# Kernel tuning notes

Hardware: AMD Instinct MI355X
Metric: run time of the kernel (lower is better)

## Reference

```python
import jax, jax.numpy as jnp
import numpy as np

D_MODEL = 768
D_STATE = 128
D_CONV = 4
EXPAND = 4
D_INNER = EXPAND * D_MODEL  # 3072
DT_RANK = 48  # ceil(768/16), mamba default dt_rank='auto'
H_MLP = 768
EPS = 1e-6


def setup_inputs() -> dict:
    key = jax.random.key(0)
    ks = jax.random.split(key, 12)
    B, T = 1, 384

    def rn(k, shape, s=0.02):
        return jax.random.normal(k, shape, jnp.float32) * s

    inp = {}
    inp["x"] = jax.random.normal(ks[0], (B, 3 * T, D_MODEL), jnp.float32)
    inp["ln_w"] = jnp.ones((6, D_MODEL), jnp.float32)  # ln1..ln6 RMSNorm weights
    # 3 independent Mamba blocks, params stacked on leading dim
    inp["in_proj_w"] = rn(ks[1], (3, 2 * D_INNER, D_MODEL))
    inp["conv_w"] = rn(ks[2], (3, D_INNER, 1, D_CONV), 0.1)  # depthwise causal conv1d
    inp["conv_b"] = rn(ks[3], (3, D_INNER), 0.1)
    inp["x_proj_w"] = rn(ks[4], (3, DT_RANK + 2 * D_STATE, D_INNER))
    inp["dt_proj_w"] = rn(ks[5], (3, D_INNER, DT_RANK), 0.1)
    inp["dt_proj_b"] = rn(ks[6], (3, D_INNER), 0.1) - 4.0  # small dt after softplus
    A = jnp.tile(jnp.arange(1, D_STATE + 1, dtype=jnp.float32)[None, None, :], (3, D_INNER, 1))
    inp["A_log"] = jnp.log(A)  # mamba S4D-real init
    inp["D_skip"] = jnp.ones((3, D_INNER), jnp.float32)
    inp["out_proj_w"] = rn(ks[7], (3, D_MODEL, D_INNER))
    # 3 GatedMLPs: fc1 -> 2*hidden (value, gate), silu gate, fc2 -> out
    inp["fc1_w"] = rn(ks[8], (3, 2 * H_MLP, D_MODEL))
    inp["fc1_b"] = jnp.zeros((3, 2 * H_MLP), jnp.float32)
    inp["fc2_w"] = rn(ks[9], (3, D_MODEL, H_MLP))
    inp["fc2_b"] = jnp.zeros((3, D_MODEL), jnp.float32)
    return inp


def _rmsnorm(x, w):
    v = jnp.mean(jnp.square(x), axis=-1, keepdims=True)
    return x * jax.lax.rsqrt(v + EPS) * w


def _mamba(u, in_w, cw, cb, xp_w, dt_w, dt_b, A_log, D_skip, out_w):
    # u: (B, T, D_MODEL)
    Bsz = u.shape[0]
    xz = u @ in_w.T  # (B,T,2*Di)
    x, z = jnp.split(xz, 2, axis=-1)
    # causal depthwise conv1d over time
    xc = jax.lax.conv_general_dilated(
        jnp.swapaxes(x, 1, 2), cw, (1,), [(D_CONV - 1, 0)],
        feature_group_count=D_INNER)  # (B,Di,T)
    x = jax.nn.silu(jnp.swapaxes(xc, 1, 2) + cb)  # (B,T,Di)
    x_dbl = x @ xp_w.T  # (B,T,dt_rank+2N)
    dt = x_dbl[..., :DT_RANK]
    Bm = x_dbl[..., DT_RANK:DT_RANK + D_STATE]
    Cm = x_dbl[..., DT_RANK + D_STATE:]
    delta = jax.nn.softplus(dt @ dt_w.T + dt_b)  # (B,T,Di)
    A = -jnp.exp(A_log)  # (Di,N)

    def step(h, inp):
        d_t, B_t, C_t, u_t = inp  # (B,Di),(B,N),(B,N),(B,Di)
        h = jnp.exp(d_t[:, :, None] * A) * h + (d_t * u_t)[:, :, None] * B_t[:, None, :]
        y = jnp.einsum('bdn,bn->bd', h, C_t)
        return h, y

    h0 = jnp.zeros((Bsz, D_INNER, D_STATE), u.dtype)
    xs = tuple(jnp.swapaxes(a, 0, 1) for a in (delta, Bm, Cm, x))  # time-major
    _, ys = jax.lax.scan(jax.checkpoint(step), h0, xs)
    y = jnp.swapaxes(ys, 0, 1) + x * D_skip  # (B,T,Di)
    return (y * jax.nn.silu(z)) @ out_w.T  # (B,T,D_MODEL)


def _gmlp(x, w1, b1, w2, b2):
    h = x @ w1.T + b1
    a, g = jnp.split(h, 2, axis=-1)
    return (jax.nn.silu(g) * a) @ w2.T + b2


def reference(x, ln_w, in_proj_w, conv_w, conv_b, x_proj_w, dt_proj_w, dt_proj_b,
              A_log, D_skip, out_proj_w, fc1_w, fc1_b, fc2_w, fc2_b):
    t = x.shape[1] // 3
    outs = []
    for i in range(3):  # music / up / down branches
        b = x[:, i * t:(i + 1) * t]
        b = b + _mamba(_rmsnorm(b, ln_w[2 * i]), in_proj_w[i], conv_w[i], conv_b[i],
                       x_proj_w[i], dt_proj_w[i], dt_proj_b[i], A_log[i], D_skip[i],
                       out_proj_w[i])
        b = b + _gmlp(_rmsnorm(b, ln_w[2 * i + 1]), fc1_w[i], fc1_b[i], fc2_w[i], fc2_b[i])
        outs.append(b)
    return jnp.concatenate(outs, axis=1)
```

## Files before the change

### kernel.cpp

```cpp
#include <hip/hip_runtime.h>
#include <hip/hip_bf16.h>

#define TSEQ 384
#define DMODEL 768
#define DINNER 3072
#define DSTATE 128
#define DTRANK 48
#define XPROJ_N (DTRANK + 2*DSTATE)
#define NSEG 3
#define LOG2E 1.44269504088896340736f
#define LN2F  0.69314718055994530942f

typedef __attribute__((ext_vector_type(8))) short short8;
typedef __attribute__((ext_vector_type(4))) float floatx4;
typedef unsigned short u16;
typedef unsigned int u32;

__device__ __forceinline__ float bf2f(u16 u) {
    return __uint_as_float(((unsigned)u) << 16);
}
__device__ __forceinline__ float ldf(const void* p, size_t i, int bf) {
    return bf ? bf2f(((const u16*)p)[i]) : ((const float*)p)[i];
}
__device__ __forceinline__ void stf(void* p, size_t i, float v, int bf) {
    if (bf) ((__hip_bfloat16*)p)[i] = __float2bfloat16(v);
    else    ((float*)p)[i] = v;
}
__device__ __forceinline__ float silu_f(float v) { return v / (1.f + __expf(-v)); }
__device__ __forceinline__ u16 f2bf(float f) {
    unsigned u = __float_as_uint(f);
    return (u16)((u + 0x7FFFu + ((u >> 16) & 1u)) >> 16);
}

__device__ __forceinline__ float exp2_fast(float x) {
#if __has_builtin(__builtin_amdgcn_exp2f)
    return __builtin_amdgcn_exp2f(x);
#else
    return exp2f(x);
#endif
}

template<int CTRL>
__device__ __forceinline__ float ror_add(float x) {
    int r = __builtin_amdgcn_update_dpp(0, __float_as_int(x), CTRL, 0xF, 0xF, true);
    return x + __int_as_float(r);
}

__device__ __forceinline__ void gl16(const void* g, void* l) {
    __builtin_amdgcn_global_load_lds(
        (const __attribute__((address_space(1))) u32*)g,
        (__attribute__((address_space(3))) u32*)l, 16, 0, 0);
}

__global__ void k_detect(const unsigned* lnw_bits, int* flag) {
    if (threadIdx.x == 0) {
        flag[0] = (lnw_bits[0] == 0x3F803F80u) ? 1 : 0;
    }
}

__global__ __launch_bounds__(256) void k_rmsnorm(
    const void* src, int src_is_f32, const void* lnw, int wbase,
    u16* out, const int* flagp)
{
    int bf  = *flagp;
    int sbf = src_is_f32 ? 0 : bf;
    int r   = blockIdx.x;
    int seg = r / TSEQ;
    int wrow = 2*seg + wbase;
    int tid = threadIdx.x;
    float v[3]; float s = 0.f;
    #pragma unroll
    for (int j = 0; j < 3; ++j) {
        int e = j*256 + tid;
        v[j] = ldf(src, (size_t)r*DMODEL + e, sbf);
        s += v[j]*v[j];
    }
    __shared__ float red[256];
    red[tid] = s; __syncthreads();
    for (int st = 128; st > 0; st >>= 1) {
        if (tid < st) red[tid] += red[tid+st];
        __syncthreads();
    }
    float rs = rsqrtf(red[0]/(float)DMODEL + 1e-6f);
    #pragma unroll
    for (int j = 0; j < 3; ++j) {
        int e = j*256 + tid;
        out[(size_t)r*DMODEL + e] = f2bf(v[j]*rs*ldf(lnw, (size_t)wrow*DMODEL + e, bf));
    }
}

__global__ __launch_bounds__(256) void k_gemm(
    const float* A, const void* W, const void* bias,
    float* C, const int* flagp, int M, int N, int K, int lda)
{
    int bf  = *flagp;
    int seg = blockIdx.z;
    int mbase = blockIdx.y * 64, nbase = blockIdx.x * 64;
    int tid = threadIdx.x;
    int tx = tid & 15, ty = tid >> 4;

    __shared__ float As[16][68];
    __shared__ float Ws[16][68];

    const float* Ag = A + (size_t)seg*M*lda;
    size_t segW = (size_t)seg*N*K;

    int lrow = tid >> 2;
    int lk   = (tid & 3) * 4;
    int wn   = nbase + lrow;

    float acc[4][4];
    #pragma unroll
    for (int i = 0; i < 4; ++i)
        #pragma unroll
        for (int j = 0; j < 4; ++j) acc[i][j] = 0.f;

    for (int kt = 0; kt < K; kt += 16) {
        float4 av = *reinterpret_cast<const float4*>(Ag + (size_t)(mbase+lrow)*lda + kt + lk);
        As[lk+0][lrow] = av.x; As[lk+1][lrow] = av.y;
        As[lk+2][lrow] = av.z; As[lk+3][lrow] = av.w;
        float w0=0.f, w1=0.f, w2=0.f, w3=0.f;
        if (wn < N) {
            size_t off = segW + (size_t)wn*K + kt + lk;
            if (bf) {
                ushort4 q = *reinterpret_cast<const ushort4*>((const u16*)W + off);
                w0 = bf2f(q.x); w1 = bf2f(q.y); w2 = bf2f(q.z); w3 = bf2f(q.w);
            } else {
                float4 f = *reinterpret_cast<const float4*>((const float*)W + off);
                w0 = f.x; w1 = f.y; w2 = f.z; w3 = f.w;
            }
        }
        Ws[lk+0][lrow] = w0; Ws[lk+1][lrow] = w1;
        Ws[lk+2][lrow] = w2; Ws[lk+3][lrow] = w3;
        __syncthreads();
        #pragma unroll
        for (int kk = 0; kk < 16; ++kk) {
            float4 a4 = *reinterpret_cast<const float4*>(&As[kk][ty*4]);
            float4 b4 = *reinterpret_cast<const float4*>(&Ws[kk][tx*4]);
            float ar[4] = {a4.x, a4.y, a4.z, a4.w};
            float br[4] = {b4.x, b4.y, b4.z, b4.w};
            #pragma unroll
            for (int i = 0; i < 4; ++i)
                #pragma unroll
                for (int j = 0; j < 4; ++j)
                    acc[i][j] = fmaf(ar[i], br[j], acc[i][j]);
        }
        __syncthreads();
    }

    #pragma unroll
    for (int i = 0; i < 4; ++i) {
        int m = mbase + ty*4 + i;
        #pragma unroll
        for (int j = 0; j < 4; ++j) {
            int n = nbase + tx*4 + j;
            if (n < N) {
                float v = acc[i][j] + ldf(bias, (size_t)seg*N + n, bf);
                v = (v > 20.f) ? v : log1pf(__expf(v));
                C[((size_t)(seg*M + m))*N + n] = v;
            }
        }
    }
}

#define LPITCH 40
__global__ __launch_bounds__(256) void k_gemm_mfma128(
    const u16* A, const void* W, u16* C, const int* flagp,
    int M, int N, int K)
{
    int bf  = *flagp;
    int seg = blockIdx.z;
    int mbase = blockIdx.y * 128, nbase = blockIdx.x * 128;
    int tid = threadIdx.x;
    int w = tid >> 6, lane = tid & 63;
    int wm = w >> 1, wn = w & 1;
    int quad = lane >> 4, l16 = lane & 15;

    __shared__ short As[128 * LPITCH];
    __shared__ short Ws[128 * LPITCH];

    const u16* Ag = A + (size_t)seg*M*K + (size_t)mbase*K;
    size_t segW = (size_t)seg*N*K;

    int sr  = tid >> 1;
    int skc = (tid & 1) * 16;

    floatx4 acc[4][4];
    #pragma unroll
    for (int i = 0; i < 4; ++i)
        #pragma unroll
        for (int j = 0; j < 4; ++j)
            acc[i][j] = (floatx4){0.f, 0.f, 0.f, 0.f};

    int wrow = nbase + sr;
    for (int kt = 0; kt < K; kt += 32) {
        const u16* ap = Ag + (size_t)sr*K + kt + skc;
        *reinterpret_cast<short8*>(&As[sr*LPITCH + skc])     = *reinterpret_cast<const short8*>(ap);
        *reinterpret_cast<short8*>(&As[sr*LPITCH + skc + 8]) = *reinterpret_cast<const short8*>(ap + 8);
        {
            short8 s0 = (short8){0,0,0,0,0,0,0,0}, s1 = s0;
            if (wrow < N) {
                size_t off = segW + (size_t)wrow*K + kt + skc;
                if (bf) {
                    s0 = *reinterpret_cast<const short8*>((const u16*)W + off);
                    s1 = *reinterpret_cast<const short8*>((const u16*)W + off + 8);
                } else {
                    const float* wp = (const float*)W + off;
                    float f[16];
                    #pragma unroll
                    for (int q = 0; q < 4; ++q) {
                        float4 v = *reinterpret_cast<const float4*>(wp + q*4);
                        f[q*4+0] = v.x; f[q*4+1] = v.y; f[q*4+2] = v.z; f[q*4+3] = v.w;
                    }
                    #pragma unroll
                    for (int q = 0; q < 8; ++q) { s0[q] = (short)f2bf(f[q]); s1[q] = (short)f2bf(f[q+8]); }
                }
            }
            *reinterpret_cast<short8*>(&Ws[sr*LPITCH + skc])     = s0;
            *reinterpret_cast<short8*>(&Ws[sr*LPITCH + skc + 8]) = s1;
        }
        __syncthreads();
        short8 af[4], bfr[4];
        #pragma unroll
        for (int i = 0; i < 4; ++i)
            af[i] = *reinterpret_cast<const short8*>(&As[(wm*64 + i*16 + l16)*LPITCH + quad*8]);
        #pragma unroll
        for (int j = 0; j < 4; ++j)
            bfr[j] = *reinterpret_cast<const short8*>(&Ws[(wn*64 + j*16 + l16)*LPITCH + quad*8]);
        #pragma unroll
        for (int i = 0; i < 4; ++i)
            #pragma unroll
            for (int j = 0; j < 4; ++j)
                acc[i][j] = __builtin_amdgcn_mfma_f32_16x16x32_bf16(af[i], bfr[j], acc[i][j], 0, 0, 0);
        __syncthreads();
    }

    #pragma unroll
    for (int i = 0; i < 4; ++i) {
        #pragma unroll
        for (int reg = 0; reg < 4; ++reg) {
            int grow = mbase + wm*64 + i*16 + quad*4 + reg;
            #pragma unroll
            for (int j = 0; j < 4; ++j) {
                int gcol = nbase + wn*64 + j*16 + l16;
                if (gcol < N)
                    C[((size_t)(seg*M + grow))*N + gcol] = f2bf(acc[i][j][reg]);
            }
        }
    }
}

#define LP2 72
__global__ __launch_bounds__(256) void k_gemm_mfma64(
    const u16* A, const void* W, const void* bias, const void* resid,
    int resid_flagged, void* C, int c_mode, const int* flagp,
    int M, int N, int K)
{
    int bf  = *flagp;
    int seg = blockIdx.z;
    int mbase = blockIdx.y * 64, nbase = blockIdx.x * 64;
    int tid = threadIdx.x;
    int w = tid >> 6, lane = tid & 63;
    int wm = w >> 1, wn = w & 1;
    int quad = lane >> 4, l16 = lane & 15;

    __shared__ short As[64 * LP2];
    __shared__ short Ws[64 * LP2];

    const u16* Ag = A + (size_t)seg*M*K + (size_t)mbase*K;
    size_t segW = (size_t)seg*N*K;

    int sr  = tid >> 2;
    int skc = (tid & 3) * 16;

    floatx4 acc[2][2];
    #pragma unroll
    for (int i = 0; i < 2; ++i)
        #pragma unroll
        for (int j = 0; j < 2; ++j)
            acc[i][j] = (floatx4){0.f, 0.f, 0.f, 0.f};

    int wrow = nbase + sr;
    for (int kt = 0; kt < K; kt += 64) {
        const u16* ap = Ag + (size_t)sr*K + kt + skc;
        *reinterpret_cast<short8*>(&As[sr*LP2 + skc])     = *reinterpret_cast<const short8*>(ap);
        *reinterpret_cast<short8*>(&As[sr*LP2 + skc + 8]) = *reinterpret_cast<const short8*>(ap + 8);
        {
            short8 s0 = (short8){0,0,0,0,0,0,0,0}, s1 = s0;
            if (wrow < N) {
                size_t off = segW + (size_t)wrow*K + kt + skc;
                if (bf) {
                    s0 = *reinterpret_cast<const short8*>((const u16*)W + off);
                    s1 = *reinterpret_cast<const short8*>((const u16*)W + off + 8);
                } else {
                    const float* wp = (const float*)W + off;
                    float f[16];
                    #pragma unroll
                    for (int q = 0; q < 4; ++q) {
                        float4 v = *reinterpret_cast<const float4*>(wp + q*4);
                        f[q*4+0] = v.x; f[q*4+1] = v.y; f[q*4+2] = v.z; f[q*4+3] = v.w;
                    }
                    #pragma unroll
                    for (int q = 0; q < 8; ++q) { s0[q] = (short)f2bf(f[q]); s1[q] = (short)f2bf(f[q+8]); }
                }
            }
            *reinterpret_cast<short8*>(&Ws[sr*LP2 + skc])     = s0;
            *reinterpret_cast<short8*>(&Ws[sr*LP2 + skc + 8]) = s1;
        }
        __syncthreads();
        #pragma unroll
        for (int kk = 0; kk < 2; ++kk) {
            short8 af[2], bfr[2];
            #pragma unroll
            for (int i = 0; i < 2; ++i)
                af[i] = *reinterpret_cast<const short8*>(&As[(wm*32 + i*16 + l16)*LP2 + kk*32 + quad*8]);
            #pragma unroll
            for (int j = 0; j < 2; ++j)
                bfr[j] = *reinterpret_cast<const short8*>(&Ws[(wn*32 + j*16 + l16)*LP2 + kk*32 + quad*8]);
            #pragma unroll
            for (int i = 0; i < 2; ++i)
                #pragma unroll
                for (int j = 0; j < 2; ++j)
                    acc[i][j] = __builtin_amdgcn_mfma_f32_16x16x32_bf16(af[i], bfr[j], acc[i][j], 0, 0, 0);
        }
        __syncthreads();
    }

    #pragma unroll
    for (int i = 0; i < 2; ++i) {
        #pragma unroll
        for (int reg = 0; reg < 4; ++reg) {
            int grow = mbase + wm*32 + i*16 + quad*4 + reg;
            #pragma unroll
            for (int j = 0; j < 2; ++j) {
                int gcol = nbase + wn*32 + j*16 + l16;
                if (gcol < N) {
                    float v = acc[i][j][reg];
                    if (bias) v += ldf(bias, (size_t)seg*N + gcol, bf);
                    size_t idx = ((size_t)(seg*M + grow))*N + gcol;
                    if (resid) v += resid_flagged ? ldf(resid, idx, bf)
                                                  : ((const float*)resid)[idx];
                    if      (c_mode == 0) ((float*)C)[idx] = v;
                    else if (c_mode == 1) ((u16*)C)[idx] = f2bf(v);
                    else                  stf(C, idx, v, bf);
                }
            }
        }
    }
}

__global__ __launch_bounds__(256) void k_fc1_gate(
    const u16* A, const void* W, const void* bias, u16* act, const int* flagp)
{
    const int M = TSEQ, K = DMODEL, NF = 2*DMODEL;
    int bf  = *flagp;
    int seg = blockIdx.z;
    int mbase = blockIdx.y * 64, nbase = blockIdx.x * 64;
    int tid = threadIdx.x;
    int w = tid >> 6, lane = tid & 63;
    int wm = w >> 1, wn = w & 1;
    int quad = lane >> 4, l16 = lane & 15;

    __shared__ short As[64 * LPITCH];
    __shared__ short Wa[64 * LPITCH];
    __shared__ short Wg[64 * LPITCH];

    const u16* Ag = A + (size_t)seg*M*K + (size_t)mbase*K;
    size_t segW = (size_t)seg*NF*K;

    int sr  = tid >> 2;
    int skc = (tid & 3) * 8;

    floatx4 acca[2][2], accg[2][2];
    #pragma unroll
    for (int i = 0; i < 2; ++i)
        #pragma unroll
        for (int j = 0; j < 2; ++j) {
            acca[i][j] = (floatx4){0.f, 0.f, 0.f, 0.f};
            accg[i][j] = (floatx4){0.f, 0.f, 0.f, 0.f};
        }

    int wra = nbase + sr;
    int wrg = nbase + DMODEL + sr;
    for (int kt = 0; kt < K; kt += 32) {
        *reinterpret_cast<short8*>(&As[sr*LPITCH + skc]) =
            *reinterpret_cast<const short8*>(Ag + (size_t)sr*K + kt + skc);
        #pragma unroll
        for (int half = 0; half < 2; ++half) {
            int wrow = half ? wrg : wra;
            short* dst = half ? Wg : Wa;
            short8 s;
            size_t off = segW + (size_t)wrow*K + kt + skc;
            if (bf) {
                s = *reinterpret_cast<const short8*>((const u16*)W + off);
            } else {
                const float* wp = (const float*)W + off;
                float4 v0 = *reinterpret_cast<const float4*>(wp);
                float4 v1 = *reinterpret_cast<const float4*>(wp + 4);
                s[0]=(short)f2bf(v0.x); s[1]=(short)f2bf(v0.y); s[2]=(short)f2bf(v0.z); s[3]=(short)f2bf(v0.w);
                s[4]=(short)f2bf(v1.x); s[5]=(short)f2bf(v1.y); s[6]=(short)f2bf(v1.z); s[7]=(short)f2bf(v1.w);
            }
            *reinterpret_cast<short8*>(&dst[sr*LPITCH + skc]) = s;
        }
        __syncthreads();
        short8 af[2], ba[2], bg[2];
        #pragma unroll
        for (int i = 0; i < 2; ++i)
            af[i] = *reinterpret_cast<const short8*>(&As[(wm*32 + i*16 + l16)*LPITCH + quad*8]);
        #pragma unroll
        for (int j = 0; j < 2; ++j) {
            ba[j] = *reinterpret_cast<const short8*>(&Wa[(wn*32 + j*16 + l16)*LPITCH + quad*8]);
            bg[j] = *reinterpret_cast<const short8*>(&Wg[(wn*32 + j*16 + l16)*LPITCH + quad*8]);
        }
        #pragma unroll
        for (int i = 0; i < 2; ++i)
            #pragma unroll
            for (int j = 0; j < 2; ++j) {
                acca[i][j] = __builtin_amdgcn_mfma_f32_16x16x32_bf16(af[i], ba[j], acca[i][j], 0, 0, 0);
                accg[i][j] = __builtin_amdgcn_mfma_f32_16x16x32_bf16(af[i], bg[j], accg[i][j], 0, 0, 0);
            }
        __syncthreads();
    }

    #pragma unroll
    for (int i = 0; i < 2; ++i) {
        #pragma unroll
        for (int reg = 0; reg < 4; ++reg) {
            int grow = mbase + wm*32 + i*16 + quad*4 + reg;
            #pragma unroll
            for (int j = 0; j < 2; ++j) {
                int gcol = nbase + wn*32 + j*16 + l16;
                float va = acca[i][j][reg] + ldf(bias, (size_t)seg*NF + gcol, bf);
                float vg = accg[i][j][reg] + ldf(bias, (size_t)seg*NF + DMODEL + gcol, bf);
                act[((size_t)(seg*M + grow))*DMODEL + gcol] = f2bf(va * silu_f(vg));
            }
        }
    }
}

__global__ __launch_bounds__(256) void k_conv(
    const u16* xz, const void* cw, const void* cb, u16* xconv, const int* flagp)
{
    int bf = *flagp;
    size_t gid = (size_t)blockIdx.x*256 + threadIdx.x;
    int d = (int)(gid % DINNER);
    size_t rt = gid / DINNER;
    int t = (int)(rt % TSEQ);
    int seg = (int)(rt / TSEQ);
    float acc = ldf(cb, (size_t)seg*DINNER + d, bf);
    const u16* xs = xz + (size_t)seg*TSEQ*(2*DINNER);
    #pragma unroll
    for (int j = 0; j < 4; ++j) {
        int ts = t - 3 + j;
        if (ts >= 0)
            acc = fmaf(ldf(cw, ((size_t)seg*DINNER + d)*4 + j, bf),
                       bf2f(xs[(size_t)ts*(2*DINNER) + d]), acc);
    }
    xconv[gid] = f2bf(silu_f(acc));
}

#define WSCH 4
#define WSCT 8
#define NPAIR (TSEQ/(2*WSCT))
#define NBX   (DINNER/WSCH)
#define GUARD_TH 0.04f

__global__ __launch_bounds__(64) void k_scan_wave(
    const float* delta, const u16* xconv, const float* xdbl, const u16* xz,
    const void* A_log, const void* D_skip, u16* yout, const int* flagp)
{
    int bf   = flagp[0];
    int seg  = blockIdx.y;
    int bx = (int)blockIdx.x;
    bx = (bx & 7) * (NBX/8) + (bx >> 3);
    int dbase = bx * WSCH;
    int lane = threadIdx.x;
    int ch = lane >> 4, sl = lane & 15;
    int d = dbase + ch;

    __shared__ float4 BUF[2][WSCT][64];
    __shared__ float  DLB2[WSCT][8];

    float a[8];
    size_t abase = ((size_t)seg*DINNER + d)*DSTATE + (size_t)sl*8;
    #pragma unroll
    for (int j = 0; j < 8; ++j)
        a[j] = -__expf(ldf(A_log, abase + j, bf)) * LOG2E;
    float gl[8]; float gmax = 0.f;
    gl[0] = 0.f;
    #pragma unroll
    for (int j = 1; j < 8; ++j) {
        gl[j] = (a[j] - a[j-1]) * LN2F;
        gmax = fmaxf(gmax, fabsf(gl[j]));
    }
    float wg = gmax;
    #pragma unroll
    for (int k = 32; k >= 1; k >>= 1) wg = fmaxf(wg, __shfl_xor(wg, k));
    float a0  = a[0];
    float Dsk = ldf(D_skip, (size_t)seg*DINNER + d, bf);
    float dskg = (sl == 0) ? Dsk : 0.f;

    const float* xdbl_s = xdbl + (size_t)seg*TSEQ*XPROJ_N;
    int loff = DTRANK + (lane & 15)*8 + ((lane >> 4) & 1)*4 + ((lane >> 5) ? DSTATE : 0);
    const float* srcl = xdbl_s + loff;

    const float* delta_s = delta + (size_t)seg*TSEQ*DINNER + dbase;
    const u16*   xconv_s = xconv + (size_t)seg*TSEQ*DINNER + dbase;
    const u16*   z_s     = xz    + (size_t)seg*TSEQ*(2*DINNER) + DINNER + dbase + ch;
    u16*         y_s     = yout  + (size_t)seg*TSEQ*DINNER + dbase + ch;

    float4  pdel = (float4){0.f, 0.f, 0.f, 0.f};
    ushort4 pu   = (ushort4){0, 0, 0, 0};
    u16     pz   = 0;

    auto STAGE = [&](int tile, int buf) {
        const float* rb = srcl + (size_t)tile*WSCT*XPROJ_N;
        #pragma unroll
        for (int t = 0; t < WSCT; ++t)
            gl16(rb + (size_t)t*XPROJ_N, &BUF[buf][t][0]);
    };
    auto PLOAD = [&](int tile) {
        if (lane < WSCT) {
            size_t ro = (size_t)(tile*WSCT + lane)*DINNER;
            pdel = *reinterpret_cast<const float4*>(delta_s + ro);
            pu   = *reinterpret_cast<const ushort4*>(xconv_s + ro);
        }
    };
    auto DSTORE = [&]() -> bool {
        if (lane < WSCT) {
            float4 w0 = (float4){pdel.x, bf2f(pu.x), pdel.y, bf2f(pu.y)};
            float4 w1 = (float4){pdel.z, bf2f(pu.z), pdel.w, bf2f(pu.w)};
            *reinterpret_cast<float4*>(&DLB2[lane][0]) = w0;
            *reinterpret_cast<float4*>(&DLB2[lane][4]) = w1;
        }
        float m4 = fmaxf(fmaxf(pdel.x, pdel.y), fmaxf(pdel.z, pdel.w));
        return __any(m4 * wg > GUARD_TH);
    };

    float h[8];
    #pragma unroll
    for (int j = 0; j < 8; ++j) h[j] = 0.f;
    float yr = 0.f;

    float2 duA, duB;
    float4 b0A, b1A, c0A, c1A;
    float4 b0B, b1B, c0B, c1B;

#define LOADOPS(BP, T, S) do {                                                \
    du##S = *reinterpret_cast<const float2*>(&DLB2[T][ch*2]);                 \
    b0##S = (BP)[(T)*64 + sl];                                                \
    b1##S = (BP)[(T)*64 + 16 + sl];                                           \
    c0##S = (BP)[(T)*64 + 32 + sl];                                           \
    c1##S = (BP)[(T)*64 + 48 + sl];                                           \
} while (0)

#define COMPUTE(S, T) do {                                                    \
    float del = du##S.x, ut = du##S.y;                                        \
    float duu = del * ut;                                                     \
    float e0,e1,e2,e3,e4,e5,e6,e7;                                            \
    if (gf) {                                                                 \
        e0 = exp2_fast(del * a0);                                             \
        e1 = e0 * fmaf(del, gl[1], 1.f);                                      \
        e2 = e1 * fmaf(del, gl[2], 1.f);                                      \
        e3 = e2 * fmaf(del, gl[3], 1.f);                                      \
        e4 = e3 * fmaf(del, gl[4], 1.f);                                      \
        e5 = e4 * fmaf(del, gl[5], 1.f);                                      \
        e6 = e5 * fmaf(del, gl[6], 1.f);                                      \
        e7 = e6 * fmaf(del, gl[7], 1.f);                                      \
    } else {                                                                  \
        e0 = exp2_fast(del*a[0]); e1 = exp2_fast(del*a[1]);                   \
        e2 = exp2_fast(del*a[2]); e3 = exp2_fast(del*a[3]);                   \
        e4 = exp2_fast(del*a[4]); e5 = exp2_fast(del*a[5]);                   \
        e6 = exp2_fast(del*a[6]); e7 = exp2_fast(del*a[7]);                   \
    }                                                                         \
    h[0] = fmaf(e0, h[0], duu*b0##S.x);                                       \
    h[1] = fmaf(e1, h[1], duu*b0##S.y);                                       \
    h[2] = fmaf(e2, h[2], duu*b0##S.z);                                       \
    h[3] = fmaf(e3, h[3], duu*b0##S.w);                                       \
    h[4] = fmaf(e4, h[4], duu*b1##S.x);                                       \
    h[5] = fmaf(e5, h[5], duu*b1##S.y);                                       \
    h[6] = fmaf(e6, h[6], duu*b1##S.z);                                       \
    h[7] = fmaf(e7, h[7], duu*b1##S.w);                                       \
    float p0 = ut * dskg;                                                     \
    p0 = fmaf(h[0], c0##S.x, p0);                                             \
    p0 = fmaf(h[1], c0##S.y, p0);                                             \
    p0 = fmaf(h[2], c0##S.z, p0);                                             \
    p0 = fmaf(h[3], c0##S.w, p0);                                             \
    float p1 = h[4]*c1##S.x;                                                  \
    p1 = fmaf(h[5], c1##S.y, p1);                                             \
    p1 = fmaf(h[6], c1##S.z, p1);                                             \
    p1 = fmaf(h[7], c1##S.w, p1);                                             \
    float p = p0 + p1;                                                        \
    p = ror_add<0x128>(p);                                                    \
    p = ror_add<0x124>(p);                                                    \
    p = ror_add<0x122>(p);                                                    \
    p = ror_add<0x121>(p);                                                    \
    if (sl == (half8 | (T))) yr = p;                                          \
} while (0)

    auto do_tile = [&](const float4* bp, bool gf, int half8) {
        LOADOPS(bp, 0, A);
        LOADOPS(bp, 1, B);
        COMPUTE(A, 0);
        LOADOPS(bp, 2, A);
        COMPUTE(B, 1);
        LOADOPS(bp, 3, B);
        COMPUTE(A, 2);
        LOADOPS(bp, 4, A);
        COMPUTE(B, 3);
        LOADOPS(bp, 5, B);
        COMPUTE(A, 4);
        LOADOPS(bp, 6, A);
        COMPUTE(B, 5);
        LOADOPS(bp, 7, B);
        COMPUTE(A, 6);
        COMPUTE(B, 7);
    };

    STAGE(0, 0);
    PLOAD(0);

    for (int p = 0; p < NPAIR; ++p) {
        int tA = 2*p;
        asm volatile("s_waitcnt vmcnt(0)" ::: "memory");
        bool exA = DSTORE();
        STAGE(tA + 1, 1);
        PLOAD(tA + 1);
        pz = z_s[(size_t)(p*16 + sl) * (size_t)(2*DINNER)];
        __builtin_amdgcn_sched_barrier(0);
        do_tile(&BUF[0][0][0], !exA, 0);
        asm volatile("s_waitcnt vmcnt(0)" ::: "memory");
        bool exB = DSTORE();
        if (tA + 2 < 2*NPAIR) {
            STAGE(tA + 2, 0);
            PLOAD(tA + 2);
        }
        __builtin_amdgcn_sched_barrier(0);
        do_tile(&BUF[1][0][0], !exB, 8);
        y_s[(size_t)(p*16 + sl) * (size_t)DINNER] = f2bf(yr * silu_f(bf2f(pz)));
        yr = 0.f;
    }
#undef LOADOPS
#undef COMPUTE
}

extern "C" void kernel_launch(void* const* d_in, const int* in_sizes, int n_in,
                              void* d_out, int out_size, void* d_ws, size_t ws_size,
                              hipStream_t stream) {
    const void* x     = d_in[0];
    const void* lnw   = d_in[1];
    const void* inw   = d_in[2];
    const void* convw = d_in[3];
    const void* convb = d_in[4];
    const void* xpw   = d_in[5];
    const void* dtw   = d_in[6];
    const void* dtb   = d_in[7];
    const void* alog  = d_in[8];
    const void* dsk   = d_in[9];
    const void* outw  = d_in[10];
    const void* fc1w  = d_in[11];
    const void* fc1b  = d_in[12];
    const void* fc2w  = d_in[13];
    const void* fc2b  = d_in[14];

    int* flag = (int*)d_ws;
    char* wsb = (char*)d_ws;
    const size_t N_U    = (size_t)NSEG*TSEQ*DMODEL;
    const size_t N_XZ   = (size_t)NSEG*TSEQ*2*DINNER;
    const size_t N_XC   = (size_t)NSEG*TSEQ*DINNER;
    const size_t N_XDBL = (size_t)NSEG*TSEQ*XPROJ_N;

    u16*   u     = (u16*)(wsb + 16);
    u16*   xz    = u + N_U;
    u16*   xconv = xz + N_XZ;
    float* xdbl  = (float*)(xconv + N_XC);
    float* delta = xdbl + N_XDBL;
    u16*   yfin  = (u16*)(delta + N_XC);
    float* b1    = (float*)(yfin + N_XC);
    u16*   actb  = (u16*)(b1 + N_U);

    k_detect<<<1, 64, 0, stream>>>((const unsigned*)lnw, flag);

    k_rmsnorm<<<NSEG*TSEQ, 256, 0, stream>>>(x, 0, lnw, 0, u, flag);
    k_gemm_mfma128<<<dim3(48, 3, NSEG), 256, 0, stream>>>(u, inw,
        xz, flag, TSEQ, 2*DINNER, DMODEL);
    k_conv<<<(NSEG*TSEQ*DINNER)/256, 256, 0, stream>>>(xz, convw, convb, xconv, flag);
    k_gemm_mfma64<<<dim3(5, 6, NSEG), 256, 0, stream>>>(xconv, xpw, nullptr, nullptr, 0,
        xdbl, 0, flag, TSEQ, XPROJ_N, DINNER);
    k_gemm<<<dim3(48, 6, NSEG), 256, 0, stream>>>(xdbl, dtw, dtb,
        delta, flag, TSEQ, DINNER, DTRANK, XPROJ_N);

    k_scan_wave<<<dim3(NBX, NSEG), 64, 0, stream>>>(
        delta, xconv, xdbl, xz, alog, dsk, yfin, flag);

    k_gemm_mfma64<<<dim3(12, 6, NSEG), 256, 0, stream>>>(yfin, outw, nullptr, x, 1,
        b1, 0, flag, TSEQ, DMODEL, DINNER);

    k_rmsnorm<<<NSEG*TSEQ, 256, 0, stream>>>(b1, 1, lnw, 1, u, flag);
    k_fc1_gate<<<dim3(12, 6, NSEG), 256, 0, stream>>>(u, fc1w, fc1b, actb, flag);
    k_gemm_mfma64<<<dim3(12, 6, NSEG), 256, 0, stream>>>(actb, fc2w, fc2b, b1, 0,
        d_out, 2, flag, TSEQ, DMODEL, DMODEL);
}
```

Baseline: 587.3 us.

## Pipeline GEMMs with direct global-to-LDS loads, XOR swizzle, and multi-buffering

Adds a new 64x64 MFMA GEMM kernel and a gated fc1 kernel. Both stage bf16 tiles straight into LDS with a gl16 helper, use an XOR-swizzled 64-wide K layout instead of padded pitch, and triple- or double-buffer tiles with explicit vmcnt waits and barriers. The in_proj GEMM moves from 128x128 tiles to the new 64x64 kernel, and the out_proj, fc1 and fc2 GEMMs switch to the pipelined versions. The goal is to overlap global memory latency with MFMA work and cut LDS bank conflicts, at the cost of more LDS per block and hand-tuned wait counts that depend on instruction ordering.

Result: faster. 551.0 us (-6.2%).

```diff
diff --git a/kernel.cpp b/kernel.cpp
--- a/kernel.cpp
+++ b/kernel.cpp
@@ -158,93 +158,6 @@
                 float v = acc[i][j] + ldf(bias, (size_t)seg*N + n, bf);
                 v = (v > 20.f) ? v : log1pf(__expf(v));
                 C[((size_t)(seg*M + m))*N + n] = v;
-            }
-        }
-    }
-}
-
-#define LPITCH 40
-__global__ __launch_bounds__(256) void k_gemm_mfma128(
-    const u16* A, const void* W, u16* C, const int* flagp,
-    int M, int N, int K)
-{
-    int bf  = *flagp;
-    int seg = blockIdx.z;
-    int mbase = blockIdx.y * 128, nbase = blockIdx.x * 128;
-    int tid = threadIdx.x;
-    int w = tid >> 6, lane = tid & 63;
-    int wm = w >> 1, wn = w & 1;
-    int quad = lane >> 4, l16 = lane & 15;
-
-    __shared__ short As[128 * LPITCH];
-    __shared__ short Ws[128 * LPITCH];
-
-    const u16* Ag = A + (size_t)seg*M*K + (size_t)mbase*K;
-    size_t segW = (size_t)seg*N*K;
-
-    int sr  = tid >> 1;
-    int skc = (tid & 1) * 16;
-
-    floatx4 acc[4][4];
-    #pragma unroll
-    for (int i = 0; i < 4; ++i)
-        #pragma unroll
-        for (int j = 0; j < 4; ++j)
-            acc[i][j] = (floatx4){0.f, 0.f, 0.f, 0.f};
-
-    int wrow = nbase + sr;
-    for (int kt = 0; kt < K; kt += 32) {
-        const u16* ap = Ag + (size_t)sr*K + kt + skc;
-        *reinterpret_cast<short8*>(&As[sr*LPITCH + skc])     = *reinterpret_cast<const short8*>(ap);
-        *reinterpret_cast<short8*>(&As[sr*LPITCH + skc + 8]) = *reinterpret_cast<const short8*>(ap + 8);
-        {
-            short8 s0 = (short8){0,0,0,0,0,0,0,0}, s1 = s0;
-            if (wrow < N) {
-                size_t off = segW + (size_t)wrow*K + kt + skc;
-                if (bf) {
-                    s0 = *reinterpret_cast<const short8*>((const u16*)W + off);
-                    s1 = *reinterpret_cast<const short8*>((const u16*)W + off + 8);
-                } else {
-                    const float* wp = (const float*)W + off;
-                    float f[16];
-                    #pragma unroll
-                    for (int q = 0; q < 4; ++q) {
-                        float4 v = *reinterpret_cast<const float4*>(wp + q*4);
-                        f[q*4+0] = v.x; f[q*4+1] = v.y; f[q*4+2] = v.z; f[q*4+3] = v.w;
-                    }
-                    #pragma unroll
-                    for (int q = 0; q < 8; ++q) { s0[q] = (short)f2bf(f[q]); s1[q] = (short)f2bf(f[q+8]); }
-                }
-            }
-            *reinterpret_cast<short8*>(&Ws[sr*LPITCH + skc])     = s0;
-            *reinterpret_cast<short8*>(&Ws[sr*LPITCH + skc + 8]) = s1;
-        }
-        __syncthreads();
-        short8 af[4], bfr[4];
-        #pragma unroll
-        for (int i = 0; i < 4; ++i)
-            af[i] = *reinterpret_cast<const short8*>(&As[(wm*64 + i*16 + l16)*LPITCH + quad*8]);
-        #pragma unroll
-        for (int j = 0; j < 4; ++j)
-            bfr[j] = *reinterpret_cast<const short8*>(&Ws[(wn*64 + j*16 + l16)*LPITCH + quad*8]);
-        #pragma unroll
-        for (int i = 0; i < 4; ++i)
-            #pragma unroll
-            for (int j = 0; j < 4; ++j)
-                acc[i][j] = __builtin_amdgcn_mfma_f32_16x16x32_bf16(af[i], bfr[j], acc[i][j], 0, 0, 0);
-        __syncthreads();
-    }
-
-    #pragma unroll
-    for (int i = 0; i < 4; ++i) {
-        #pragma unroll
-        for (int reg = 0; reg < 4; ++reg) {
-            int grow = mbase + wm*64 + i*16 + quad*4 + reg;
-            #pragma unroll
-            for (int j = 0; j < 4; ++j) {
-                int gcol = nbase + wn*64 + j*16 + l16;
-                if (gcol < N)
-                    C[((size_t)(seg*M + grow))*N + gcol] = f2bf(acc[i][j][reg]);
             }
         }
     }
@@ -349,7 +262,139 @@
     }
 }
 
-__global__ __launch_bounds__(256) void k_fc1_gate(
+__global__ __launch_bounds__(256) void k_gemm_mfma64g(
+    const u16* A, const void* W, const void* bias, const void* resid,
+    int resid_flagged, void* C, int c_mode, const int* flagp,
+    int M, int N, int K)
+{
+    int bf  = *flagp;
+    int seg = blockIdx.z;
+    int mbase = blockIdx.y * 64, nbase = blockIdx.x * 64;
+    int tid = threadIdx.x;
+    int w = tid >> 6, lane = tid & 63;
+    int wm = w >> 1, wn = w & 1;
+    int quad = lane >> 4, l16 = lane & 15;
+
+    __shared__ short As[3][64*64];
+    __shared__ short Ws[3][64*64];
+
+    const u16* Ag  = A + (size_t)seg*M*K + (size_t)mbase*K;
+    const u16* Wgp = (const u16*)W + (size_t)seg*N*K + (size_t)nbase*K;
+    int nk = K >> 6;
+
+    int srow = lane >> 3;
+    int scol = ((lane & 7) ^ srow) * 8;
+    int swz  = (l16 & 7) * 8;
+
+    floatx4 acc[2][2];
+    #pragma unroll
+    for (int i = 0; i < 2; ++i)
+        #pragma unroll
+        for (int j = 0; j < 2; ++j)
+            acc[i][j] = (floatx4){0.f, 0.f, 0.f, 0.f};
+
+    auto CMP = [&](int b) {
+        #pragma unroll
+        for (int kk = 0; kk < 2; ++kk) {
+            short8 af[2], bfr[2];
+            #pragma unroll
+            for (int i = 0; i < 2; ++i) {
+                int row = wm*32 + i*16 + l16;
+                af[i] = *reinterpret_cast<const short8*>(
+                    &As[b][row*64 + (((kk*4 + quad)*8) ^ swz)]);
+            }
+            #pragma unroll
+            for (int j = 0; j < 2; ++j) {
+                int row = wn*32 + j*16 + l16;
+                bfr[j] = *reinterpret_cast<const short8*>(
+                    &Ws[b][row*64 + (((kk*4 + quad)*8) ^ swz)]);
+            }
+            #pragma unroll
+            for (int i = 0; i < 2; ++i)
+                #pragma unroll
+                for (int j = 0; j < 2; ++j)
+                    acc[i][j] = __builtin_amdgcn_mfma_f32_16x16x32_bf16(af[i], bfr[j], acc[i][j], 0, 0, 0);
+        }
+    };
+
+    if (bf) {
+        auto STG = [&](int t, int b) {
+            size_t kt = (size_t)t << 6;
+            #pragma unroll
+            for (int i8 = 0; i8 < 2; ++i8) {
+                int rbase = w*16 + i8*8;
+                gl16(Ag  + (size_t)(rbase + srow)*K + kt + scol, &As[b][rbase*64]);
+                gl16(Wgp + (size_t)(rbase + srow)*K + kt + scol, &Ws[b][rbase*64]);
+            }
+        };
+        STG(0, 0);
+        STG(1, 1);
+        for (int t = 0; t < nk - 2; ++t) {
+            STG(t + 2, (t + 2) % 3);
+            asm volatile("s_waitcnt vmcnt(8)" ::: "memory");
+            __builtin_amdgcn_s_barrier();
+            __builtin_amdgcn_sched_barrier(0);
+            CMP(t % 3);
+            asm volatile("" ::: "memory");
+            __builtin_amdgcn_s_barrier();
+        }
+        asm volatile("s_waitcnt vmcnt(4)" ::: "memory");
+        __builtin_amdgcn_s_barrier();
+        __builtin_amdgcn_sched_barrier(0);
+        CMP((nk - 2) % 3);
+        asm volatile("" ::: "memory");
+        __builtin_amdgcn_s_barrier();
+        asm volatile("s_waitcnt vmcnt(0)" ::: "memory");
+        __builtin_amdgcn_s_barrier();
+        __builtin_amdgcn_sched_barrier(0);
+        CMP((nk - 1) % 3);
+    } else {
+        const float* Wf = (const float*)W + (size_t)seg*N*K + (size_t)nbase*K;
+        int row2 = tid >> 2;
+        for (int t = 0; t < nk; ++t) {
+            size_t kt = (size_t)t << 6;
+            #pragma unroll
+            for (int i8 = 0; i8 < 2; ++i8) {
+                int rbase = w*16 + i8*8;
+                gl16(Ag + (size_t)(rbase + srow)*K + kt + scol, &As[0][rbase*64]);
+            }
+            const float* wp = Wf + (size_t)row2*K + kt;
+            #pragma unroll
+            for (int h2 = 0; h2 < 2; ++h2) {
+                int gs = (tid & 3) + h2*4;
+                short8 s;
+                #pragma unroll
+                for (int q2 = 0; q2 < 8; ++q2) s[q2] = (short)f2bf(wp[gs*8 + q2]);
+                *reinterpret_cast<short8*>(&Ws[0][row2*64 + ((gs ^ (row2 & 7)) * 8)]) = s;
+            }
+            __syncthreads();
+            CMP(0);
+            __syncthreads();
+        }
+    }
+
+    #pragma unroll
+    for (int i = 0; i < 2; ++i) {
+        #pragma unroll
+        for (int reg = 0; reg < 4; ++reg) {
+            int grow = mbase + wm*32 + i*16 + quad*4 + reg;
+            #pragma unroll
+            for (int j = 0; j < 2; ++j) {
+                int gcol = nbase + wn*32 + j*16 + l16;
+                float v = acc[i][j][reg];
+                if (bias) v += ldf(bias, (size_t)seg*N + gcol, bf);
+                size_t idx = ((size_t)(seg*M + grow))*N + gcol;
+                if (resid) v += resid_flagged ? ldf(resid, idx, bf)
+                                              : ((const float*)resid)[idx];
+                if      (c_mode == 0) ((float*)C)[idx] = v;
+                else if (c_mode == 1) ((u16*)C)[idx] = f2bf(v);
+                else                  stf(C, idx, v, bf);
+            }
+        }
+    }
+}
+
+__global__ __launch_bounds__(256) void k_fc1_gate_g(
     const u16* A, const void* W, const void* bias, u16* act, const int* flagp)
 {
     const int M = TSEQ, K = DMODEL, NF = 2*DMODEL;
@@ -361,15 +406,18 @@
     int wm = w >> 1, wn = w & 1;
     int quad = lane >> 4, l16 = lane & 15;
 
-    __shared__ short As[64 * LPITCH];
-    __shared__ short Wa[64 * LPITCH];
-    __shared__ short Wg[64 * LPITCH];
-
-    const u16* Ag = A + (size_t)seg*M*K + (size_t)mbase*K;
-    size_t segW = (size_t)seg*NF*K;
-
-    int sr  = tid >> 2;
-    int skc = (tid & 3) * 8;
+    __shared__ short As[2][64*64];
+    __shared__ short Wa[2][64*64];
+    __shared__ short Wg[2][64*64];
+
+    const u16* Ag  = A + (size_t)seg*M*K + (size_t)mbase*K;
+    const u16* Wap = (const u16*)W + (size_t)seg*NF*K + (size_t)nbase*K;
+    const u16* Wgp = Wap + (size_t)DMODEL*K;
+    int nk = K >> 6;
+
+    int srow = lane >> 3;
+    int scol = ((lane & 7) ^ srow) * 8;
+    int swz  = (l16 & 7) * 8;
 
     floatx4 acca[2][2], accg[2][2];
     #pragma unroll
@@ -380,46 +428,86 @@
             accg[i][j] = (floatx4){0.f, 0.f, 0.f, 0.f};
         }
 
-    int wra = nbase + sr;
-    int wrg = nbase + DMODEL + sr;
-    for (int kt = 0; kt < K; kt += 32) {
-        *reinterpret_cast<short8*>(&As[sr*LPITCH + skc]) =
-            *reinterpret_cast<const short8*>(Ag + (size_t)sr*K + kt + skc);
-        #pragma unroll
-        for (int half = 0; half < 2; ++half) {
-            int wrow = half ? wrg : wra;
-            short* dst = half ? Wg : Wa;
-            short8 s;
-            size_t off = segW + (size_t)wrow*K + kt + skc;
-            if (bf) {
-                s = *reinterpret_cast<const short8*>((const u16*)W + off);
-            } else {
-                const float* wp = (const float*)W + off;
-                float4 v0 = *reinterpret_cast<const float4*>(wp);
-                float4 v1 = *reinterpret_cast<const float4*>(wp + 4);
-                s[0]=(short)f2bf(v0.x); s[1]=(short)f2bf(v0.y); s[2]=(short)f2bf(v0.z); s[3]=(short)f2bf(v0.w);
-                s[4]=(short)f2bf(v1.x); s[5]=(short)f2bf(v1.y); s[6]=(short)f2bf(v1.z); s[7]=(short)f2bf(v1.w);
-            }
-            *reinterpret_cast<short8*>(&dst[sr*LPITCH + skc]) = s;
-        }
-        __syncthreads();
-        short8 af[2], ba[2], bg[2];
-        #pragma unroll
-        for (int i = 0; i < 2; ++i)
-            af[i] = *reinterpret_cast<const short8*>(&As[(wm*32 + i*16 + l16)*LPITCH + quad*8]);
-        #pragma unroll
-        for (int j = 0; j < 2; ++j) {
-            ba[j] = *reinterpret_cast<const short8*>(&Wa[(wn*32 + j*16 + l16)*LPITCH + quad*8]);
-            bg[j] = *reinterpret_cast<const short8*>(&Wg[(wn*32 + j*16 + l16)*LPITCH + quad*8]);
-        }
-        #pragma unroll
-        for (int i = 0; i < 2; ++i)
+    auto CMP = [&](int b) {
+        #pragma unroll
+        for (int kk = 0; kk < 2; ++kk) {
+            short8 af[2], ba[2], bg[2];
+            #pragma unroll
+            for (int i = 0; i < 2; ++i) {
+                int row = wm*32 + i*16 + l16;
+                af[i] = *reinterpret_cast<const short8*>(
+                    &As[b][row*64 + (((kk*4 + quad)*8) ^ swz)]);
+            }
             #pragma unroll
             for (int j = 0; j < 2; ++j) {
-                acca[i][j] = __builtin_amdgcn_mfma_f32_16x16x32_bf16(af[i], ba[j], acca[i][j], 0, 0, 0);
-                accg[i][j] = __builtin_amdgcn_mfma_f32_16x16x32_bf16(af[i], bg[j], accg[i][j], 0, 0, 0);
-            }
-        __syncthreads();
+                int row = wn*32 + j*16 + l16;
+                int col = ((kk*4 + quad)*8) ^ swz;
+                ba[j] = *reinterpret_cast<const short8*>(&Wa[b][row*64 + col]);
+                bg[j] = *reinterpret_cast<const short8*>(&Wg[b][row*64 + col]);
+            }
+            #pragma unroll
+            for (int i = 0; i < 2; ++i)
+                #pragma unroll
+                for (int j = 0; j < 2; ++j) {
+                    acca[i][j] = __builtin_amdgcn_mfma_f32_16x16x32_bf16(af[i], ba[j], acca[i][j], 0, 0, 0);
+                    accg[i][j] = __builtin_amdgcn_mfma_f32_16x16x32_bf16(af[i], bg[j], accg[i][j], 0, 0, 0);
+                }
+        }
+    };
+
+    if (bf) {
+        auto STG = [&](int t, int b) {
+            size_t kt = (size_t)t << 6;
+            #pragma unroll
+            for (int i8 = 0; i8 < 2; ++i8) {
+                int rbase = w*16 + i8*8;
+                size_t so = (size_t)(rbase + srow)*K + kt + scol;
+                gl16(Ag  + so, &As[b][rbase*64]);
+                gl16(Wap + so, &Wa[b][rbase*64]);
+                gl16(Wgp + so, &Wg[b][rbase*64]);
+            }
+        };
+        STG(0, 0);
+        for (int t = 0; t < nk - 1; ++t) {
+            STG(t + 1, (t + 1) & 1);
+            asm volatile("s_waitcnt vmcnt(6)" ::: "memory");
+            __builtin_amdgcn_s_barrier();
+            __builtin_amdgcn_sched_barrier(0);
+            CMP(t & 1);
+            asm volatile("" ::: "memory");
+            __builtin_amdgcn_s_barrier();
+        }
+        asm volatile("s_waitcnt vmcnt(0)" ::: "memory");
+        __builtin_amdgcn_s_barrier();
+        __builtin_amdgcn_sched_barrier(0);
+        CMP((nk - 1) & 1);
+    } else {
+        const float* Waf = (const float*)W + (size_t)seg*NF*K + (size_t)nbase*K;
+        const float* Wgf = Waf + (size_t)DMODEL*K;
+        int row2 = tid >> 2;
+        for (int t = 0; t < nk; ++t) {
+            size_t kt = (size_t)t << 6;
+            #pragma unroll
+            for (int i8 = 0; i8 < 2; ++i8) {
+                int rbase = w*16 + i8*8;
+                gl16(Ag + (size_t)(rbase + srow)*K + kt + scol, &As[0][rbase*64]);
+            }
+            #pragma unroll
+            for (int h2 = 0; h2 < 2; ++h2) {
+                int gs = (tid & 3) + h2*4;
+                int wcol = (gs ^ (row2 & 7)) * 8;
+                short8 sa, sg;
+                const float* wpa = Waf + (size_t)row2*K + kt + gs*8;
+                const float* wpg = Wgf + (size_t)row2*K + kt + gs*8;
+                #pragma unroll
+                for (int q2 = 0; q2 < 8; ++q2) { sa[q2] = (short)f2bf(wpa[q2]); sg[q2] = (short)f2bf(wpg[q2]); }
+                *reinterpret_cast<short8*>(&Wa[0][row2*64 + wcol]) = sa;
+                *reinterpret_cast<short8*>(&Wg[0][row2*64 + wcol]) = sg;
+            }
+            __syncthreads();
+            CMP(0);
+            __syncthreads();
+        }
     }
 
     #pragma unroll
@@ -682,8 +770,8 @@
     k_detect<<<1, 64, 0, stream>>>((const unsigned*)lnw, flag);
 
     k_rmsnorm<<<NSEG*TSEQ, 256, 0, stream>>>(x, 0, lnw, 0, u, flag);
-    k_gemm_mfma128<<<dim3(48, 3, NSEG), 256, 0, stream>>>(u, inw,
-        xz, flag, TSEQ, 2*DINNER, DMODEL);
+    k_gemm_mfma64g<<<dim3(96, 6, NSEG), 256, 0, stream>>>(u, inw, nullptr, nullptr, 0,
+        xz, 1, flag, TSEQ, 2*DINNER, DMODEL);
     k_conv<<<(NSEG*TSEQ*DINNER)/256, 256, 0, stream>>>(xz, convw, convb, xconv, flag);
     k_gemm_mfma64<<<dim3(5, 6, NSEG), 256, 0, stream>>>(xconv, xpw, nullptr, nullptr, 0,
         xdbl, 0, flag, TSEQ, XPROJ_N, DINNER);
@@ -693,11 +781,11 @@
     k_scan_wave<<<dim3(NBX, NSEG), 64, 0, stream>>>(
         delta, xconv, xdbl, xz, alog, dsk, yfin, flag);
 
-    k_gemm_mfma64<<<dim3(12, 6, NSEG), 256, 0, stream>>>(yfin, outw, nullptr, x, 1,
+    k_gemm_mfma64g<<<dim3(12, 6, NSEG), 256, 0, stream>>>(yfin, outw, nullptr, x, 1,
         b1, 0, flag, TSEQ, DMODEL, DINNER);
 
     k_rmsnorm<<<NSEG*TSEQ, 256, 0, stream>>>(b1, 1, lnw, 1, u, flag);
-    k_fc1_gate<<<dim3(12, 6, NSEG), 256, 0, stream>>>(u, fc1w, fc1b, actb, flag);
-    k_gemm_mfma64<<<dim3(12, 6, NSEG), 256, 0, stream>>>(actb, fc2w, fc2b, b1, 0,
+    k_fc1_gate_g<<<dim3(12, 6, NSEG), 256, 0, stream>>>(u, fc1w, fc1b, actb, flag);
+    k_gemm_mfma64g<<<dim3(12, 6, NSEG), 256, 0, stream>>>(actb, fc2w, fc2b, b1, 0,
         d_out, 2, flag, TSEQ, DMODEL, DMODEL);
 }
```
